# Optimization experiments

Hardware: AMD Instinct MI355X
Metric: run time of the kernel (lower is better)

## Reference

```python
import jax, jax.numpy as jnp
import numpy as np

WS = 7          # window size (square)
SS = 3          # shift size
NH = 6          # num heads
EPS = 1e-5      # LayerNorm eps (torch default)


def _ln(x, g, b):
    m = jnp.mean(x, axis=-1, keepdims=True)
    v = jnp.mean(jnp.square(x - m), axis=-1, keepdims=True)
    return (x - m) * jax.lax.rsqrt(v + EPS) * g + b


def _window_partition(x):
    # (B,H,W,C) -> (B*nW, WS*WS, C)
    B, H, W, C = x.shape
    x = x.reshape(B, H // WS, WS, W // WS, WS, C)
    return x.transpose(0, 1, 3, 2, 4, 5).reshape(-1, WS * WS, C)


def _window_reverse(w, B, H, W):
    C = w.shape[-1]
    x = w.reshape(B, H // WS, W // WS, WS, WS, C)
    return x.transpose(0, 1, 3, 2, 4, 5).reshape(B, H, W, C)


def _make_rpi():
    coords = np.stack(np.meshgrid(np.arange(WS), np.arange(WS), indexing='ij'))  # (2,WS,WS)
    cf = coords.reshape(2, -1)
    rel = cf[:, :, None] - cf[:, None, :]            # (2,N,N)
    rel = rel.transpose(1, 2, 0).astype(np.int64)
    rel[..., 0] += WS - 1
    rel[..., 1] += WS - 1
    rel[..., 0] *= 2 * WS - 1
    return rel.sum(-1)                               # (N,N)


def _make_mask(H, W):
    # standard shifted-window attention mask, values in {0, -100}
    img = np.zeros((H, W), dtype=np.float32)
    cnt = 0
    for hs in (slice(0, -WS), slice(-WS, -SS), slice(-SS, None)):
        for ws_ in (slice(0, -WS), slice(-WS, -SS), slice(-SS, None)):
            img[hs, ws_] = cnt
            cnt += 1
    win = img.reshape(H // WS, WS, W // WS, WS).transpose(0, 2, 1, 3).reshape(-1, WS * WS)
    diff = win[:, None, :] - win[:, :, None]
    return np.where(diff != 0, np.float32(-100.0), np.float32(0.0))  # (nW,N,N)


def setup_inputs() -> dict:
    key = jax.random.key(0)
    ks = jax.random.split(key, 8)
    B, H, W, C = 16, 112, 112, 192
    Dh = C * 4
    s = 0.02
    inp = {
        'x': jax.random.normal(ks[0], (B, H, W, C), jnp.float32),
        'mask_matrix': jnp.asarray(_make_mask(H, W)),
        'rpi': jnp.asarray(_make_rpi(), jnp.int32),
        'rpb_table': s * jax.random.normal(ks[1], ((2 * WS - 1) ** 2, NH), jnp.float32),
        'norm1_g': jnp.ones((C,), jnp.float32),
        'norm1_b': jnp.zeros((C,), jnp.float32),
        'qkv_w': s * jax.random.normal(ks[2], (3 * C, C), jnp.float32),
        'qkv_b': jnp.zeros((3 * C,), jnp.float32),
        'proj_w': s * jax.random.normal(ks[3], (C, C), jnp.float32),
        'proj_b': jnp.zeros((C,), jnp.float32),
        'norm2_g': jnp.ones((C,), jnp.float32),
        'norm2_b': jnp.zeros((C,), jnp.float32),
        'fc1_w': s * jax.random.normal(ks[4], (Dh, C), jnp.float32),
        'fc1_b': jnp.zeros((Dh,), jnp.float32),
        'fc2_w': s * jax.random.normal(ks[5], (C, Dh), jnp.float32),
        'fc2_b': jnp.zeros((C,), jnp.float32),
    }
    return inp


def reference(x, mask_matrix, rpi, rpb_table, norm1_g, norm1_b, qkv_w, qkv_b,
              proj_w, proj_b, norm2_g, norm2_b, fc1_w, fc1_b, fc2_w, fc2_b):
    B, H, W, C = x.shape
    N = WS * WS
    hd = C // NH
    scale = hd ** -0.5

    shortcut = x
    xn = _ln(x, norm1_g, norm1_b)
    shifted = jnp.roll(xn, shift=(-SS, -SS), axis=(1, 2))

    xw = _window_partition(shifted)                          # (B_, N, C)
    B_ = xw.shape[0]
    qkv = xw @ qkv_w.T + qkv_b                               # (B_, N, 3C)
    qkv = qkv.reshape(B_, N, 3, NH, hd).transpose(2, 0, 3, 1, 4)
    q, k, v = qkv[0] * scale, qkv[1], qkv[2]                 # (B_, NH, N, hd)

    attn = jnp.einsum('bhnd,bhmd->bhnm', q, k)               # (B_, NH, N, N)
    bias = rpb_table[rpi.reshape(-1)].reshape(N, N, NH).transpose(2, 0, 1)
    attn = attn + bias[None]

    nW = mask_matrix.shape[0]
    attn = attn.reshape(B_ // nW, nW, NH, N, N) + mask_matrix[None, :, None]
    attn = jax.nn.softmax(attn.reshape(B_, NH, N, N), axis=-1)

    out = jnp.einsum('bhnm,bhmd->bhnd', attn, v)             # (B_, NH, N, hd)
    out = out.transpose(0, 2, 1, 3).reshape(B_, N, C)
    out = out @ proj_w.T + proj_b

    shifted = _window_reverse(out, B, H, W)
    xa = jnp.roll(shifted, shift=(SS, SS), axis=(1, 2))
    x = shortcut + xa

    h = _ln(x, norm2_g, norm2_b)
    h = jax.nn.gelu(h @ fc1_w.T + fc1_b, approximate=False)
    h = h @ fc2_w.T + fc2_b
    return x + h
```

## Files before the change

### kernel.cpp

```cpp
#include <hip/hip_runtime.h>
#include <hip/hip_bf16.h>

typedef __hip_bfloat16 bf16;
typedef __attribute__((ext_vector_type(8))) short bh8;
typedef __attribute__((ext_vector_type(4))) short bh4;
typedef __attribute__((ext_vector_type(4))) float f4;

#define TOKENS 200704
#define CDIM   192

__device__ __forceinline__ void gload16(const bf16* g, bf16* l) {
    __builtin_amdgcn_global_load_lds((const __attribute__((address_space(1))) void*)g,
                                     (__attribute__((address_space(3))) void*)l,
                                     16, 0, 0);
}
#define MFMA __builtin_amdgcn_mfma_f32_16x16x32_bf16

__device__ __forceinline__ void stv(float* p, float v) { *p = v; }
__device__ __forceinline__ void stv(bf16* p, float v)  { *p = __float2bfloat16(v); }
__device__ __forceinline__ short f2bs(float v) {
    bf16 h = __float2bfloat16(v); return *(short*)&h;
}

__device__ __forceinline__ int row2tok(int row) {
    int win = row / 49, n = row - win * 49;
    int b = win >> 8, rem = win & 255;
    int hs = (rem >> 4) * 7 + n / 7;
    int wsx = (rem & 15) * 7 + n % 7;
    int hh = hs + 3; if (hh >= 112) hh -= 112;
    int ww = wsx + 3; if (ww >= 112) ww -= 112;
    return (b * 112 + hh) * 112 + ww;
}

__global__ void cvt_all(const float* __restrict__ a, const float* __restrict__ b,
                        const float* __restrict__ c, const float* __restrict__ d,
                        bf16* __restrict__ dst) {
    int i = blockIdx.x * 256 + threadIdx.x;
    if (i >= 442368) return;
    float v;
    if (i < 110592)       v = a[i];
    else if (i < 147456)  v = b[i - 110592];
    else if (i < 294912)  v = c[i - 147456];
    else                  v = d[i - 294912];
    dst[i] = __float2bfloat16(v);
}

__global__ void bmp_kernel(const int* __restrict__ rpi, const float* __restrict__ tab,
                           const float* __restrict__ mask, float* __restrict__ bmp) {
    int idx = blockIdx.x * 256 + threadIdx.x;
    if (idx >= 98304) return;
    int cls = idx / 24576, rem = idx - cls * 24576;
    int h = rem >> 12, qk = rem & 4095;
    int qq = qk >> 6, kk = qk & 63;
    float v;
    if (kk >= 49) v = -1e30f;
    else if (qq >= 49) v = 0.f;
    else {
        int rep = ((cls & 2) ? 240 : 0) + ((cls & 1) ? 15 : 0);
        v = tab[rpi[qq * 49 + kk] * 6 + h] + mask[rep * 2401 + qq * 49 + kk];
    }
    bmp[idx] = v;
}

template<int GATHER>
__global__ __launch_bounds__(256)
void ln_kernel(const float* __restrict__ src, const float* __restrict__ gw,
               const float* __restrict__ bw, bf16* __restrict__ dst) {
    const int lane = threadIdx.x & 63;
    const int gwv  = (blockIdx.x * 256 + threadIdx.x) >> 6;
    const int nwv  = (gridDim.x * 256) >> 6;
    const float g0 = gw[lane], g1 = gw[lane + 64], g2 = gw[lane + 128];
    const float b0 = bw[lane], b1 = bw[lane + 64], b2 = bw[lane + 128];
    for (int row = gwv; row < TOKENS; row += nwv) {
        const float* p = GATHER ? src + (size_t)row2tok(row) * CDIM
                                : src + (size_t)row * CDIM;
        float v0 = p[lane], v1 = p[lane + 64], v2 = p[lane + 128];
        float s = v0 + v1 + v2;
        float q = v0 * v0 + v1 * v1 + v2 * v2;
        #pragma unroll
        for (int o = 32; o; o >>= 1) { s += __shfl_xor(s, o, 64); q += __shfl_xor(q, o, 64); }
        float mean = s * (1.f / 192.f);
        float var  = q * (1.f / 192.f) - mean * mean;
        float rstd = rsqrtf(var + 1e-5f);
        bf16* d = dst + (size_t)row * CDIM;
        d[lane]       = __float2bfloat16((v0 - mean) * rstd * g0 + b0);
        d[lane + 64]  = __float2bfloat16((v1 - mean) * rstd * g1 + b1);
        d[lane + 128] = __float2bfloat16((v2 - mean) * rstd * g2 + b2);
    }
}

template<int EPI, int FUSELN, typename OutT>
__global__ __launch_bounds__(256)
void gemm_bt(const bf16* __restrict__ A, const bf16* __restrict__ W,
             const float* __restrict__ bias, OutT* out,
             const float* res, int N, int K,
             const float* __restrict__ g2, const float* __restrict__ b2g,
             bf16* __restrict__ hbuf) {
    __shared__ __align__(16) bf16 As[128 * 32];
    __shared__ __align__(16) bf16 Bs[192 * 32];
    __shared__ float rsum[FUSELN ? 128 : 1][2], rsq[FUSELN ? 128 : 1][2];
    const int tid = threadIdx.x, wid = tid >> 6, lane = tid & 63;
    const int mbase = blockIdx.y * 128, nbase = blockIdx.x * 192;
    const int wm = wid >> 1, wn = wid & 1;
    const int r = lane & 15, q = lane >> 4;
    const int sx = (q ^ ((r >> 1) & 3)) << 3;
    const bf16* Ab = A + (size_t)mbase * K;
    const bf16* Wb = W + (size_t)nbase * K;
    f4 acc[4][6] = {};
    const int cbase = wid * 64 + lane;
    for (int k0 = 0; k0 < K; k0 += 32) {
        #pragma unroll
        for (int p = 0; p < 2; ++p) {
            int ci = p * 256 + cbase;
            int row = ci >> 2, g = (ci & 3) ^ ((row >> 1) & 3);
            gload16(Ab + (size_t)row * K + (k0 + (g << 3)),
                    &As[(p * 256 + wid * 64) * 8]);
        }
        #pragma unroll
        for (int p = 0; p < 3; ++p) {
            int ci = p * 256 + cbase;
            int row = ci >> 2, g = (ci & 3) ^ ((row >> 1) & 3);
            gload16(Wb + (size_t)row * K + (k0 + (g << 3)),
                    &Bs[(p * 256 + wid * 64) * 8]);
        }
        __syncthreads();
        bh8 af[4], bfr[6];
        #pragma unroll
        for (int i = 0; i < 4; ++i)
            af[i] = *(const bh8*)&As[(wm * 64 + i * 16 + r) * 32 + sx];
        #pragma unroll
        for (int j = 0; j < 6; ++j)
            bfr[j] = *(const bh8*)&Bs[(wn * 96 + j * 16 + r) * 32 + sx];
        #pragma unroll
        for (int i = 0; i < 4; ++i)
            #pragma unroll
            for (int j = 0; j < 6; ++j)
                acc[i][j] = MFMA(af[i], bfr[j], acc[i][j], 0, 0, 0);
        __syncthreads();
    }
    const int cr = q, cc = r;
    if constexpr (EPI == 0) {
        #pragma unroll
        for (int i = 0; i < 4; ++i)
            #pragma unroll
            for (int j = 0; j < 6; ++j) {
                int ncol = nbase + wn * 96 + j * 16 + cc;
                float bv = bias[ncol];
                #pragma unroll
                for (int rr = 0; rr < 4; ++rr) {
                    int row = mbase + wm * 64 + i * 16 + cr * 4 + rr;
                    stv(&out[(size_t)row * N + ncol], acc[i][j][rr] + bv);
                }
            }
    } else {
        #pragma unroll
        for (int i = 0; i < 4; ++i) {
            size_t dstRow[4];
            float ps[4], pq[4];
            #pragma unroll
            for (int rr = 0; rr < 4; ++rr) {
                int row = mbase + wm * 64 + i * 16 + cr * 4 + rr;
                dstRow[rr] = (size_t)row2tok(row) * CDIM;
                ps[rr] = 0.f; pq[rr] = 0.f;
            }
            #pragma unroll
            for (int j = 0; j < 6; ++j) {
                int ncol = nbase + wn * 96 + j * 16 + cc;
                float bv = bias[ncol];
                #pragma unroll
                for (int rr = 0; rr < 4; ++rr) {
                    float v = acc[i][j][rr] + bv + res[dstRow[rr] + ncol];
                    stv(&out[dstRow[rr] + ncol], v);
                    acc[i][j][rr] = v;
                    ps[rr] += v; pq[rr] += v * v;
                }
            }
            if constexpr (FUSELN) {
                #pragma unroll
                for (int rr = 0; rr < 4; ++rr) {
                    float s = ps[rr], qq = pq[rr];
                    #pragma unroll
                    for (int o = 1; o < 16; o <<= 1) { s += __shfl_xor(s, o, 64); qq += __shfl_xor(qq, o, 64); }
                    if (cc == 0) {
                        int rl = wm * 64 + i * 16 + cr * 4 + rr;
                        rsum[rl][wn] = s; rsq[rl][wn] = qq;
                    }
                }
            }
        }
        if constexpr (FUSELN) {
            __syncthreads();
            #pragma unroll
            for (int i = 0; i < 4; ++i) {
                size_t dstRow[4];
                float mean[4], rstd[4];
                #pragma unroll
                for (int rr = 0; rr < 4; ++rr) {
                    int rl = wm * 64 + i * 16 + cr * 4 + rr;
                    dstRow[rr] = (size_t)row2tok(mbase + rl) * CDIM;
                    float m = (rsum[rl][0] + rsum[rl][1]) * (1.f / 192.f);
                    float var = (rsq[rl][0] + rsq[rl][1]) * (1.f / 192.f) - m * m;
                    mean[rr] = m; rstd[rr] = rsqrtf(var + 1e-5f);
                }
                #pragma unroll
                for (int j = 0; j < 6; ++j) {
                    int ncol = nbase + wn * 96 + j * 16 + cc;
                    float gv = g2[ncol], bvv = b2g[ncol];
                    #pragma unroll
                    for (int rr = 0; rr < 4; ++rr)
                        hbuf[dstRow[rr] + ncol] =
                            __float2bfloat16((acc[i][j][rr] - mean[rr]) * rstd[rr] * gv + bvv);
                }
            }
        }
    }
}

__global__ __launch_bounds__(384, 2)
void qkvattn_kernel(const bf16* __restrict__ xw, const bf16* __restrict__ wq,
                    const float* __restrict__ qkvb, const float* __restrict__ bmp,
                    bf16* __restrict__ attno) {
    __shared__ __align__(16) bf16 xsf[6][64][32];
    __shared__ __align__(16) bf16 qk[6][2][64][32];
    const int tid = threadIdx.x, h = tid >> 6, lane = tid & 63;
    const int r = lane & 15, q = lane >> 4;
    const int win = blockIdx.x;
    const int sxk = (q ^ ((r >> 1) & 3)) << 3;

    #pragma unroll
    for (int it = 0; it < 4; ++it) {
        int l = it * 384 + tid;
        int ks = l >> 8, rem = l & 255, tok = rem >> 2;
        int kg = (rem & 3) ^ ((tok >> 1) & 3);
        int srow = win * 49 + tok; if (srow > 200703) srow = 200703;
        gload16(xw + (size_t)srow * 192 + ks * 32 + kg * 8,
                &xsf[0][0][0] + (size_t)l * 8);
    }
    __syncthreads();
    f4 aqk[4][4] = {}, av[4][2] = {};
    for (int ks = 0; ks < 6; ++ks) {
        bh8 wqk[4], wv[2], xf[4];
        #pragma unroll
        for (int i = 0; i < 4; ++i)
            wqk[i] = *(const bh8*)&wq[(size_t)((i >> 1) * 192 + h * 32 + (i & 1) * 16 + r) * 192 + ks * 32 + q * 8];
        #pragma unroll
        for (int jv = 0; jv < 2; ++jv)
            wv[jv] = *(const bh8*)&wq[(size_t)(384 + h * 32 + jv * 16 + r) * 192 + ks * 32 + q * 8];
        #pragma unroll
        for (int mt = 0; mt < 4; ++mt)
            xf[mt] = *(const bh8*)&xsf[ks][mt * 16 + r][sxk];
        #pragma unroll
        for (int i = 0; i < 4; ++i)
            #pragma unroll
            for (int jn = 0; jn < 4; ++jn)
                aqk[i][jn] = MFMA(wqk[i], xf[jn], aqk[i][jn], 0, 0, 0);
        #pragma unroll
        for (int mt = 0; mt < 4; ++mt)
            #pragma unroll
            for (int jv = 0; jv < 2; ++jv)
                av[mt][jv] = MFMA(xf[mt], wv[jv], av[mt][jv], 0, 0, 0);
    }
    __syncthreads();
    bf16* qkh = &qk[h][0][0][0];
    #pragma unroll
    for (int i = 0; i < 4; ++i) {
        const int t = i >> 1;
        const f4 bz = *(const f4*)&qkvb[t * 192 + h * 32 + (i & 1) * 16 + q * 4];
        const float sc = (i < 2) ? 0.17677669529663689f : 1.0f;
        #pragma unroll
        for (int jn = 0; jn < 4; ++jn) {
            const int tok = jn * 16 + r;
            bh4 w;
            #pragma unroll
            for (int rr = 0; rr < 4; ++rr)
                w[rr] = f2bs((aqk[i][jn][rr] + bz[rr]) * sc);
            const int g = (((i & 1) * 4 + q) ^ ((tok & 3) << 1));
            *(bh4*)&qkh[(t * 64 + tok) * 32 + g * 4] = w;
        }
    }
    bf16* vth = &xsf[0][0][0] + h * 2048;
    #pragma unroll
    for (int jv = 0; jv < 2; ++jv) {
        const float bv = qkvb[384 + h * 32 + jv * 16 + r];
        const int d = jv * 16 + r;
        #pragma unroll
        for (int mt = 0; mt < 4; ++mt) {
            bh4 w;
            #pragma unroll
            for (int rr = 0; rr < 4; ++rr)
                w[rr] = f2bs(av[mt][jv][rr] + bv);
            const int g = ((mt * 4 + q) ^ ((r & 7) << 1));
            *(bh4*)&vth[d * 64 + g * 4] = w;
        }
    }
    f4 as[4][4] = {};
    {
        const int sl = ((2 * q) ^ ((r & 3) << 1)) << 2;
        bh8 kf[4], qf[4];
        #pragma unroll
        for (int mt = 0; mt < 4; ++mt)
            kf[mt] = *(const bh8*)&qkh[(64 + mt * 16 + r) * 32 + sl];
        #pragma unroll
        for (int jn = 0; jn < 4; ++jn)
            qf[jn] = *(const bh8*)&qkh[(jn * 16 + r) * 32 + sl];
        #pragma unroll
        for (int mt = 0; mt < 4; ++mt)
            #pragma unroll
            for (int jn = 0; jn < 4; ++jn)
                as[mt][jn] = MFMA(kf[mt], qf[jn], as[mt][jn], 0, 0, 0);
    }
    const int rem = win & 255;
    const int cls = (((rem >> 4) == 15) ? 2 : 0) + (((rem & 15) == 15) ? 1 : 0);
    const float* bmh = bmp + ((size_t)(cls * 6 + h) << 12);
    #pragma unroll
    for (int jn = 0; jn < 4; ++jn) {
        const int qq = jn * 16 + r;
        #pragma unroll
        for (int mt = 0; mt < 4; ++mt) {
            const f4 b = *(const f4*)&bmh[qq * 64 + mt * 16 + q * 4];
            #pragma unroll
            for (int rr = 0; rr < 4; ++rr) as[mt][jn][rr] += b[rr];
        }
    }
    float inv4[4];
    #pragma unroll
    for (int jn = 0; jn < 4; ++jn) {
        float mx = -1e30f;
        #pragma unroll
        for (int mt = 0; mt < 4; ++mt)
            #pragma unroll
            for (int rr = 0; rr < 4; ++rr) mx = fmaxf(mx, as[mt][jn][rr]);
        mx = fmaxf(mx, __shfl_xor(mx, 16, 64));
        mx = fmaxf(mx, __shfl_xor(mx, 32, 64));
        float sm = 0.f;
        #pragma unroll
        for (int mt = 0; mt < 4; ++mt)
            #pragma unroll
            for (int rr = 0; rr < 4; ++rr) {
                float e = __expf(as[mt][jn][rr] - mx);
                as[mt][jn][rr] = e; sm += e;
            }
        sm += __shfl_xor(sm, 16, 64);
        sm += __shfl_xor(sm, 32, 64);
        inv4[jn] = __builtin_amdgcn_rcpf(sm);
    }
    #pragma unroll
    for (int jn = 0; jn < 4; ++jn) {
        const int qq = jn * 16 + r;
        #pragma unroll
        for (int mt = 0; mt < 4; ++mt) {
            bh4 w;
            #pragma unroll
            for (int rr = 0; rr < 4; ++rr) w[rr] = f2bs(as[mt][jn][rr] * inv4[jn]);
            const int g = ((mt * 4 + q) ^ ((r & 7) << 1));
            *(bh4*)&qkh[qq * 64 + g * 4] = w;
        }
    }
    f4 ao[4][2] = {};
    #pragma unroll
    for (int k2 = 0; k2 < 2; ++k2) {
        const int sl = ((k2 * 8 + 2 * q) ^ ((r & 7) << 1)) << 2;
        bh8 pf[4], vf[2];
        #pragma unroll
        for (int mt = 0; mt < 4; ++mt)
            pf[mt] = *(const bh8*)&qkh[(mt * 16 + r) * 64 + sl];
        #pragma unroll
        for (int jv = 0; jv < 2; ++jv)
            vf[jv] = *(const bh8*)&vth[(jv * 16 + r) * 64 + sl];
        #pragma unroll
        for (int mt = 0; mt < 4; ++mt)
            #pragma unroll
            for (int jv = 0; jv < 2; ++jv)
                ao[mt][jv] = MFMA(pf[mt], vf[jv], ao[mt][jv], 0, 0, 0);
    }
    #pragma unroll
    for (int mt = 0; mt < 4; ++mt)
        #pragma unroll
        for (int jv = 0; jv < 2; ++jv) {
            const int d = jv * 16 + r;
            #pragma unroll
            for (int rr = 0; rr < 4; ++rr) {
                const int qq = mt * 16 + q * 4 + rr;
                if (qq < 49)
                    attno[((size_t)win * 49 + qq) * 192 + h * 32 + d] =
                        __float2bfloat16(ao[mt][jv][rr]);
            }
        }
}

__global__ __launch_bounds__(256, 4)
void mlp_kernel(const bf16* __restrict__ Aht, const bf16* __restrict__ w1,
                const float* __restrict__ b1, const bf16* __restrict__ w2,
                const float* __restrict__ b2, float* __restrict__ out) {
    __shared__ __align__(16) bf16 As[6][64][32];
    __shared__ __align__(16) bf16 Hs[2][64][64];
    const int tid = threadIdx.x, wid = tid >> 6, lane = tid & 63;
    const int mbase = blockIdx.x * 64;
    const int r = lane & 15, q = lane >> 4, ko = q * 8;
    const int sxA = (q ^ ((r >> 1) & 3)) << 3;
    #pragma unroll
    for (int it = 0; it < 6; ++it) {
        int l = it * 256 + wid * 64 + lane;
        int ks = l >> 8, rem2 = l & 255, row = rem2 >> 2;
        int g = (rem2 & 3) ^ ((row >> 1) & 3);
        gload16(Aht + (size_t)(mbase + row) * 192 + ks * 32 + g * 8,
                &As[0][0][0] + (size_t)(it * 256 + wid * 64) * 8);
    }
    __syncthreads();
    f4 acc2[4][3] = {};
    for (int c = 0; c < 12; ++c) {
        const int cb = c * 64;
        bh8 w1f[6];
        #pragma unroll
        for (int ks = 0; ks < 6; ++ks)
            w1f[ks] = *(const bh8*)&w1[(size_t)(cb + wid * 16 + r) * 192 + ks * 32 + ko];
        f4 acc1[4] = {};
        #pragma unroll
        for (int ks = 0; ks < 6; ++ks)
            #pragma unroll
            for (int i = 0; i < 4; ++i) {
                bh8 af = *(const bh8*)(&As[ks][0][0] + (i * 16 + r) * 32 + sxA);
                acc1[i] = MFMA(af, w1f[ks], acc1[i], 0, 0, 0);
            }
        bh8 w2f[2][3];
        #pragma unroll
        for (int k2 = 0; k2 < 2; ++k2)
            #pragma unroll
            for (int j = 0; j < 3; ++j)
                w2f[k2][j] = *(const bh8*)&w2[(size_t)(wid * 48 + j * 16 + r) * 768 + cb + k2 * 32 + ko];
        const float b1v = b1[cb + wid * 16 + r];
        bf16 (*Hp)[64] = Hs[c & 1];
        #pragma unroll
        for (int i = 0; i < 4; ++i) {
            #pragma unroll
            for (int rr = 0; rr < 4; ++rr) {
                int row = i * 16 + q * 4 + rr;
                int col = wid * 16 + r;
                float v = acc1[i][rr] + b1v;
                float u = v * (1.5957691216f + 0.0713548162f * v * v);
                float en = __expf(-u);
                float t = __builtin_amdgcn_rcpf(1.f + en);
                Hp[row][(((col >> 3) ^ (row & 7)) << 3) | (col & 7)] =
                    __float2bfloat16(v * t);
            }
        }
        __syncthreads();
        #pragma unroll
        for (int k2 = 0; k2 < 2; ++k2)
            #pragma unroll
            for (int i = 0; i < 4; ++i) {
                int row = i * 16 + r;
                bh8 af = *(const bh8*)(&Hp[row][0] + ((((k2 * 4 + q) ^ (row & 7)) & 7) << 3));
                #pragma unroll
                for (int j = 0; j < 3; ++j)
                    acc2[i][j] = MFMA(af, w2f[k2][j], acc2[i][j], 0, 0, 0);
            }
    }
    #pragma unroll
    for (int i = 0; i < 4; ++i)
        #pragma unroll
        for (int j = 0; j < 3; ++j) {
            int ncol = wid * 48 + j * 16 + r;
            float bv = b2[ncol];
            #pragma unroll
            for (int rr = 0; rr < 4; ++rr) {
                size_t idx = (size_t)(mbase + i * 16 + q * 4 + rr) * 192 + ncol;
                out[idx] = acc2[i][j][rr] + bv + out[idx];
            }
        }
}

extern "C" void kernel_launch(void* const* d_in, const int* in_sizes, int n_in,
                              void* d_out, int out_size, void* d_ws, size_t ws_size,
                              hipStream_t stream) {
    const float* x     = (const float*)d_in[0];
    const float* mask  = (const float*)d_in[1];
    const int*   rpi   = (const int*)d_in[2];
    const float* rpb   = (const float*)d_in[3];
    const float* n1g   = (const float*)d_in[4];
    const float* n1b   = (const float*)d_in[5];
    const float* qkvw  = (const float*)d_in[6];
    const float* qkvb  = (const float*)d_in[7];
    const float* projw = (const float*)d_in[8];
    const float* projb = (const float*)d_in[9];
    const float* n2g   = (const float*)d_in[10];
    const float* n2b   = (const float*)d_in[11];
    const float* fc1w  = (const float*)d_in[12];
    const float* fc1b  = (const float*)d_in[13];
    const float* fc2w  = (const float*)d_in[14];
    const float* fc2b  = (const float*)d_in[15];

    char* ws = (char*)d_ws;
    bf16*  attno  = (bf16*)ws;
    float* bmp    = (float*)(ws + 77070336);
    bf16*  wq     = (bf16*)(ws + 77463552);
    bf16*  wp     = (bf16*)(ws + 77684736);
    bf16*  w1     = (bf16*)(ws + 77758464);
    bf16*  w2     = (bf16*)(ws + 78053376);
    bf16*  xw     = (bf16*)d_out;
    float* x1     = (float*)d_out;

    const bool fuse = ws_size >= 155418624ull;
    bf16* hbuf = fuse ? (bf16*)(ws + 78348288) : (bf16*)ws;

    cvt_all<<<1728, 256, 0, stream>>>(qkvw, projw, fc1w, fc2w, wq);
    bmp_kernel<<<384, 256, 0, stream>>>(rpi, rpb, mask, bmp);

    ln_kernel<1><<<2048, 256, 0, stream>>>(x, n1g, n1b, xw);
    qkvattn_kernel<<<4096, 384, 0, stream>>>(xw, wq, qkvb, bmp, attno);
    if (fuse) {
        gemm_bt<1, 1, float><<<dim3(1, 1568), 256, 0, stream>>>(
            attno, wp, projb, x1, x, 192, 192, n2g, n2b, hbuf);
    } else {
        gemm_bt<1, 0, float><<<dim3(1, 1568), 256, 0, stream>>>(
            attno, wp, projb, x1, x, 192, 192, nullptr, nullptr, nullptr);
        ln_kernel<0><<<2048, 256, 0, stream>>>(x1, n2g, n2b, hbuf);
    }
    mlp_kernel<<<3136, 256, 0, stream>>>(hbuf, w1, fc1b, w2, fc2b, (float*)d_out);
}
```

Before: 731.3 us.

## Fuse LayerNorm1 and window gather into the QKV-attention kernel

Removes the separate ln_kernel pass that wrote normalized, window-partitioned bf16 activations to a scratch buffer. The attention kernel now reads fp32 x rows directly through row2tok, computes mean/rstd with wavefront shuffles, and writes the swizzled bf16 tile into LDS. This drops one kernel launch and a full write plus read of the intermediate tensor. In exchange it gives up async global-to-LDS loads, holds 33 floats per thread in registers, and reads fp32 instead of bf16 inside the kernel.

```diff
diff --git a/kernel.cpp b/kernel.cpp
--- a/kernel.cpp
+++ b/kernel.cpp
@@ -217,7 +217,9 @@
 }
 
 __global__ __launch_bounds__(384, 2)
-void qkvattn_kernel(const bf16* __restrict__ xw, const bf16* __restrict__ wq,
+void qkvattn_kernel(const float* __restrict__ xg, const float* __restrict__ n1g,
+                    const float* __restrict__ n1b,
+                    const bf16* __restrict__ wq,
                     const float* __restrict__ qkvb, const float* __restrict__ bmp,
                     bf16* __restrict__ attno) {
     __shared__ __align__(16) bf16 xsf[6][64][32];
@@ -226,15 +228,44 @@
     const int r = lane & 15, q = lane >> 4;
     const int win = blockIdx.x;
     const int sxk = (q ^ ((r >> 1) & 3)) << 3;
-
-    #pragma unroll
-    for (int it = 0; it < 4; ++it) {
-        int l = it * 384 + tid;
-        int ks = l >> 8, rem = l & 255, tok = rem >> 2;
-        int kg = (rem & 3) ^ ((tok >> 1) & 3);
-        int srow = win * 49 + tok; if (srow > 200703) srow = 200703;
-        gload16(xw + (size_t)srow * 192 + ks * 32 + kg * 8,
-                &xsf[0][0][0] + (size_t)l * 8);
+    bf16* xsf0 = &xsf[0][0][0];
+
+    {
+        const float g0 = n1g[lane], g1 = n1g[lane + 64], g2 = n1g[lane + 128];
+        const float b0 = n1b[lane], b1 = n1b[lane + 64], b2 = n1b[lane + 128];
+        float rv[11][3];
+        #pragma unroll
+        for (int t = 0; t < 11; ++t) {
+            int tok = h + t * 6;
+            if (tok < 64) {
+                int wrow = win * 49 + (tok < 49 ? tok : 48);
+                const float* p = xg + (size_t)row2tok(wrow) * 192;
+                rv[t][0] = p[lane]; rv[t][1] = p[lane + 64]; rv[t][2] = p[lane + 128];
+            }
+        }
+        #pragma unroll
+        for (int t = 0; t < 11; ++t) {
+            int tok = h + t * 6;
+            if (tok < 64) {
+                float v0 = rv[t][0], v1 = rv[t][1], v2 = rv[t][2];
+                float s = v0 + v1 + v2;
+                float qs = v0 * v0 + v1 * v1 + v2 * v2;
+                #pragma unroll
+                for (int o = 32; o; o >>= 1) { s += __shfl_xor(s, o, 64); qs += __shfl_xor(qs, o, 64); }
+                float mean = s * (1.f / 192.f);
+                float rstd = rsqrtf(qs * (1.f / 192.f) - mean * mean + 1e-5f);
+                float ov[3] = { (v0 - mean) * rstd * g0 + b0,
+                                (v1 - mean) * rstd * g1 + b1,
+                                (v2 - mean) * rstd * g2 + b2 };
+                #pragma unroll
+                for (int c = 0; c < 3; ++c) {
+                    int k = lane + 64 * c;
+                    int ks = k >> 5, g = (k >> 3) & 3;
+                    int slot = g ^ ((tok >> 1) & 3);
+                    xsf0[ks * 2048 + tok * 32 + slot * 8 + (k & 7)] = __float2bfloat16(ov[c]);
+                }
+            }
+        }
     }
     __syncthreads();
     f4 aqk[4][4] = {}, av[4][2] = {};
@@ -278,7 +309,7 @@
             *(bh4*)&qkh[(t * 64 + tok) * 32 + g * 4] = w;
         }
     }
-    bf16* vth = &xsf[0][0][0] + h * 2048;
+    bf16* vth = xsf0 + h * 2048;
     #pragma unroll
     for (int jv = 0; jv < 2; ++jv) {
         const float bv = qkvb[384 + h * 32 + jv * 16 + r];
@@ -497,7 +528,6 @@
     bf16*  wp     = (bf16*)(ws + 77684736);
     bf16*  w1     = (bf16*)(ws + 77758464);
     bf16*  w2     = (bf16*)(ws + 78053376);
-    bf16*  xw     = (bf16*)d_out;
     float* x1     = (float*)d_out;
 
     const bool fuse = ws_size >= 155418624ull;
@@ -506,8 +536,7 @@
     cvt_all<<<1728, 256, 0, stream>>>(qkvw, projw, fc1w, fc2w, wq);
     bmp_kernel<<<384, 256, 0, stream>>>(rpi, rpb, mask, bmp);
 
-    ln_kernel<1><<<2048, 256, 0, stream>>>(x, n1g, n1b, xw);
-    qkvattn_kernel<<<4096, 384, 0, stream>>>(xw, wq, qkvb, bmp, attno);
+    qkvattn_kernel<<<4096, 384, 0, stream>>>(x, n1g, n1b, wq, qkvb, bmp, attno);
     if (fuse) {
         gemm_bt<1, 1, float><<<dim3(1, 1568), 256, 0, stream>>>(
             attno, wp, projb, x1, x, 192, 192, n2g, n2b, hbuf);
```

Result: slower. 757.0 us (+3.5%).
